# Optimization experiments

Measured on AMD Instinct MI355X. Metric: run time of the kernel, lower is better.

## Reference

```python
import jax, jax.numpy as jnp
import numpy as np

TOP_K = 4

def setup_inputs() -> dict:
    key = jax.random.key(0)
    ks = jax.random.split(key, 10)
    s = 0.02
    return {
        "x": jax.random.normal(ks[0], (4, 1024, 2048), jnp.float32),
        "expert_bias": jnp.zeros((64,), jnp.float32),
        "router_w": jax.random.normal(ks[1], (64, 2048), jnp.float32) * s,
        "gate_w": jax.random.normal(ks[2], (8192, 2048), jnp.float32) * s,
        "up_w": jax.random.normal(ks[3], (8192, 2048), jnp.float32) * s,
        "down_w": jax.random.normal(ks[4], (2048, 8192), jnp.float32) * s,
        "w_down": jax.random.normal(ks[5], (512, 2048), jnp.float32) * s,
        "w_up": jax.random.normal(ks[6], (2048, 512), jnp.float32) * s,
        "experts_w12": jax.random.normal(ks[7], (64, 512, 2048), jnp.float32) * s,
        "experts_w3": jax.random.normal(ks[8], (64, 1024, 512), jnp.float32) * s,
    }


def reference(x, expert_bias, router_w, gate_w, up_w, down_w, w_down, w_up, experts_w12, experts_w3):
    B, S, D = x.shape
    E = router_w.shape[0]
    K = TOP_K
    h = x.reshape(-1, D)            # [N, D]
    N = h.shape[0]
    NK = N * K

    # --- router (fp32) ---
    logits = h @ router_w.T          # [N, E]
    scores = jax.nn.sigmoid(logits)
    z_loss = jnp.mean(logits * logits) * 1e-4
    sel = scores + expert_bias
    _, topk_idx = jax.lax.top_k(sel, K)                      # [N, K]
    topk_logits = jnp.take_along_axis(logits, topk_idx, axis=1)
    gating = jax.nn.softmax(topk_logits, axis=-1)            # [N, K]

    # --- shared SwiGLU expert ---
    shared = (jax.nn.silu(h @ gate_w.T) * (h @ up_w.T)) @ down_w.T   # [N, D]

    # --- bottleneck down projection ---
    hd = h @ w_down.T                # [N, bottle]
    Bn = hd.shape[1]

    # --- dispatch: sort tokens by expert, capacity max_load per expert ---
    flat = topk_idx.reshape(-1)                      # [NK]
    perm = jnp.argsort(flat)                         # stable sort
    sorted_e = flat[perm]
    counts = jnp.bincount(flat, length=E)
    ptr = jnp.cumsum(counts) - counts                # start offset per expert
    local = jnp.arange(NK) - ptr[sorted_e]           # rank within expert
    max_load = (NK // E // 8 + 6) * 8                # static python int
    num_slots = E * max_load
    mask = local < max_load
    slots = sorted_e * max_load + local
    tok = jnp.repeat(jnp.arange(N), K)               # token id per routed slot

    # reverse_map[slot] = token index (N = dummy)
    rm = jnp.full((num_slots + 1,), N, dtype=jnp.int32)
    rm = rm.at[jnp.where(mask, slots, num_slots)].set(tok[perm].astype(jnp.int32))
    reverse_map = rm[:num_slots]

    hwd = jnp.concatenate([hd, jnp.zeros((1, Bn), hd.dtype)], axis=0)
    padding = hwd[reverse_map].reshape(E, max_load, Bn)

    # --- grouped expert GEMMs ---
    h12 = jnp.einsum('emb,ebf->emf', padding, experts_w12)   # [E, L, 2*F]
    h1, h2 = jnp.split(h12, 2, axis=-1)
    pout = jnp.einsum('emf,efb->emb', jax.nn.silu(h1) * h2, experts_w3)
    pout = pout.reshape(-1, Bn)                              # [num_slots, bottle]

    # --- combine: gather back per (token, k) slot and mix with gating ---
    powd = jnp.concatenate([pout, jnp.zeros((1, Bn), pout.dtype)], axis=0)
    gm = jnp.full((NK + 1,), num_slots, dtype=jnp.int32)
    gm = gm.at[jnp.where(mask, perm, NK)].set(jnp.where(mask, slots, num_slots).astype(jnp.int32))
    gather_map = gm[:NK]
    gathered = powd[gather_map].reshape(N, K, Bn)
    routed_b = jnp.einsum('nk,nkb->nb', gating, gathered)
    routed = routed_b @ w_up.T                               # [N, D]

    # eval mode: route_scale = 1.0, moe_scale = 0.5 (one shared expert), aux_loss = 0
    out = (shared + routed) * 0.5
    return out.reshape(B, S, D), z_loss
```

## Files before the change

kernel.cpp:

```cpp
#include <hip/hip_runtime.h>
#include <math.h>

#define NTOK 4096
#define DMODEL 2048
#define ENUM 64
#define HSH 8192
#define BND 512
#define FEXP 1024
#define MAXL 304
#define EPAD 384
#define ECH 16

typedef float f32x4 __attribute__((ext_vector_type(4)));
using bf16x8 = __attribute__((ext_vector_type(8))) __bf16;

typedef const __attribute__((address_space(1))) unsigned int cgu32;
typedef __attribute__((address_space(3))) unsigned int lu32;
#define GLOAD16(g, l) __builtin_amdgcn_global_load_lds((cgu32*)(g), (lu32*)(l), 16, 0, 0)

__device__ __forceinline__ unsigned short f2bf(float f) {
    union { float f; unsigned int u; } v; v.f = f;
    unsigned int u = v.u;
    return (unsigned short)((u + 0x7FFFu + ((u >> 16) & 1u)) >> 16);
}
__device__ __forceinline__ float bf2f(unsigned short s) {
    union { unsigned int u; float f; } v; v.u = ((unsigned int)s) << 16;
    return v.f;
}

__global__ __launch_bounds__(256) void init_kernel(float* zacc, int* slot2tok, unsigned short* hdz) {
    int i = blockIdx.x * 256 + threadIdx.x;
    if (i == 0) *zacc = 0.f;
    if (i < ENUM * MAXL) slot2tok[i] = NTOK;
    if (i < BND) hdz[i] = 0;
}

__global__ __launch_bounds__(256) void convert_kernel(
    const float* __restrict__ in, unsigned short* __restrict__ out, long long n)
{
    long long stride = (long long)gridDim.x * 256 * 8;
    for (long long i = ((long long)blockIdx.x * 256 + threadIdx.x) * 8; i < n; i += stride) {
        float4 a = *(const float4*)(in + i);
        float4 b = *(const float4*)(in + i + 4);
        union { unsigned short s[8]; uint4 v; } o;
        o.s[0] = f2bf(a.x); o.s[1] = f2bf(a.y); o.s[2] = f2bf(a.z); o.s[3] = f2bf(a.w);
        o.s[4] = f2bf(b.x); o.s[5] = f2bf(b.y); o.s[6] = f2bf(b.z); o.s[7] = f2bf(b.w);
        *(uint4*)(out + i) = o.v;
    }
}

__global__ __launch_bounds__(256) void convert_x_kernel(
    const float* __restrict__ in, unsigned short* __restrict__ hi,
    unsigned short* __restrict__ lo, long long n)
{
    long long stride = (long long)gridDim.x * 256 * 8;
    for (long long i = ((long long)blockIdx.x * 256 + threadIdx.x) * 8; i < n; i += stride) {
        float4 a = *(const float4*)(in + i);
        float4 b = *(const float4*)(in + i + 4);
        union { unsigned short s[8]; uint4 v; } oh, ol;
        float f[8] = {a.x, a.y, a.z, a.w, b.x, b.y, b.z, b.w};
#pragma unroll
        for (int j = 0; j < 8; j++) {
            unsigned short h = f2bf(f[j]);
            oh.s[j] = h;
            ol.s[j] = f2bf(f[j] - bf2f(h));
        }
        *(uint4*)(hi + i) = oh.v;
        *(uint4*)(lo + i) = ol.v;
    }
}

__global__ __launch_bounds__(256) void convert_rw_kernel(
    const float* __restrict__ rw, unsigned short* __restrict__ whi,
    unsigned short* __restrict__ wlo)
{
    int i = (blockIdx.x * 256 + threadIdx.x) * 4;
    if (i >= 128 * 2048) return;
    ushort4 oh = {0, 0, 0, 0}, ol = {0, 0, 0, 0};
    if (i < 64 * 2048) {
        float4 f = *(const float4*)(rw + i);
        float v[4] = {f.x, f.y, f.z, f.w};
        unsigned short h;
        h = f2bf(v[0]); oh.x = h; ol.x = f2bf(v[0] - bf2f(h));
        h = f2bf(v[1]); oh.y = h; ol.y = f2bf(v[1] - bf2f(h));
        h = f2bf(v[2]); oh.z = h; ol.z = f2bf(v[2] - bf2f(h));
        h = f2bf(v[3]); oh.w = h; ol.w = f2bf(v[3] - bf2f(h));
    }
    *(ushort4*)(whi + i) = oh;
    *(ushort4*)(wlo + i) = ol;
}

__global__ __launch_bounds__(256) void tconv_kernel(
    const float* __restrict__ in, unsigned short* __restrict__ out, int Kd, int Nd)
{
    __shared__ float t[32][33];
    size_t zoff = (size_t)blockIdx.z * Kd * Nd;
    in += zoff; out += zoff;
    int n0 = blockIdx.x * 32, k0 = blockIdx.y * 32;
    int r = threadIdx.x >> 3, c = (threadIdx.x & 7) * 4;
    float4 v = *(const float4*)(in + (size_t)(k0 + r) * Nd + n0 + c);
    t[r][c] = v.x; t[r][c + 1] = v.y; t[r][c + 2] = v.z; t[r][c + 3] = v.w;
    __syncthreads();
    ushort4 o;
    o.x = f2bf(t[c + 0][r]); o.y = f2bf(t[c + 1][r]);
    o.z = f2bf(t[c + 2][r]); o.w = f2bf(t[c + 3][r]);
    *(ushort4*)(out + (size_t)(n0 + r) * Kd + k0 + c) = o;
}

__global__ __launch_bounds__(256) void rgemm_kernel(
    const unsigned short* __restrict__ xb, const unsigned short* __restrict__ xlo,
    const unsigned short* __restrict__ whi, const unsigned short* __restrict__ wlo,
    float* __restrict__ logits)
{
    __shared__ unsigned short As[2][128 * 64];
    __shared__ unsigned short Bs[2][128 * 64];
    const int z = blockIdx.z;
    const int m0 = blockIdx.y * 128;
    const int tid = threadIdx.x;
    const int lane = tid & 63;
    const int w = tid >> 6;
    const int wm = (w >> 1) * 64;
    const int wn = (w & 1) * 64;

    const unsigned short* Ab = (z == 2) ? xlo : xb;
    const unsigned short* Bb = (z == 1) ? wlo : whi;
    float* Cb = logits + (size_t)z * NTOK * 128;

    size_t asrc[4], bsrc[4];
    int ldso[4];
#pragma unroll
    for (int i = 0; i < 4; i++) {
        int u = i * 256 + tid;
        int r = u >> 3;
        int ce = ((u & 7) ^ (r & 7)) * 8;
        ldso[i] = u * 8;
        asrc[i] = (size_t)(m0 + r) * DMODEL + ce;
        bsrc[i] = (size_t)r * DMODEL + ce;
    }

    const int lrow = lane & 15;
    const int kg = lane >> 4;
    const int mk = (lrow & 7) << 4;
    int arx[4], brx[4];
#pragma unroll
    for (int t = 0; t < 4; t++) {
        arx[t] = (wm + t * 16 + lrow) * 128;
        brx[t] = (wn + t * 16 + lrow) * 128;
    }

    f32x4 acc[4][4];
#pragma unroll
    for (int a = 0; a < 4; a++)
#pragma unroll
        for (int b = 0; b < 4; b++) acc[a][b] = (f32x4)0.f;

#pragma unroll
    for (int i = 0; i < 4; i++) GLOAD16(Ab + asrc[i], &As[0][ldso[i]]);
#pragma unroll
    for (int i = 0; i < 4; i++) GLOAD16(Bb + bsrc[i], &Bs[0][ldso[i]]);
#pragma unroll
    for (int i = 0; i < 4; i++) GLOAD16(Ab + asrc[i] + 64, &As[1][ldso[i]]);
#pragma unroll
    for (int i = 0; i < 4; i++) GLOAD16(Bb + bsrc[i] + 64, &Bs[1][ldso[i]]);

    const int nt = DMODEL >> 6;
    int cur = 0;
    for (int t = 0; t < nt; ++t) {
        if (t + 1 < nt) asm volatile("s_waitcnt vmcnt(8)" ::: "memory");
        else            asm volatile("s_waitcnt vmcnt(0)" ::: "memory");
        __builtin_amdgcn_s_barrier();
        __builtin_amdgcn_sched_barrier(0);
        const char* Abase = (const char*)&As[cur][0];
        const char* Bbase = (const char*)&Bs[cur][0];
#pragma unroll
        for (int ks = 0; ks < 2; ks++) {
            const int cb = (ks * 64 + kg * 16) ^ mk;
            bf16x8 a[4], b[4];
#pragma unroll
            for (int t2 = 0; t2 < 4; t2++) {
                a[t2] = *(const bf16x8*)(Abase + arx[t2] + cb);
                b[t2] = *(const bf16x8*)(Bbase + brx[t2] + cb);
            }
#pragma unroll
            for (int ni = 0; ni < 4; ni++)
#pragma unroll
                for (int mi = 0; mi < 4; mi++)
                    acc[mi][ni] = __builtin_amdgcn_mfma_f32_16x16x32_bf16(a[mi], b[ni], acc[mi][ni], 0, 0, 0);
        }
        __builtin_amdgcn_sched_barrier(0);
        asm volatile("s_waitcnt lgkmcnt(0)" ::: "memory");
        __builtin_amdgcn_s_barrier();
        __builtin_amdgcn_sched_barrier(0);
        const int kn = (t + 2) * 64;
        if (kn < DMODEL) {
#pragma unroll
            for (int i = 0; i < 4; i++) GLOAD16(Ab + asrc[i] + kn, &As[cur][ldso[i]]);
#pragma unroll
            for (int i = 0; i < 4; i++) GLOAD16(Bb + bsrc[i] + kn, &Bs[cur][ldso[i]]);
        }
        cur ^= 1;
    }

    const int rb0 = m0 + wm + (kg << 2);
#pragma unroll
    for (int mi = 0; mi < 4; mi++)
#pragma unroll
        for (int ni = 0; ni < 4; ni++) {
            int col = wn + ni * 16 + lrow;
#pragma unroll
            for (int r = 0; r < 4; r++)
                Cb[(size_t)(rb0 + mi * 16 + r) * 128 + col] = acc[mi][ni][r];
        }
}

__global__ __launch_bounds__(256) void topk_kernel(
    const float* __restrict__ logits, const float* __restrict__ bias,
    int* __restrict__ topk_idx, float* __restrict__ gating, float* __restrict__ zacc)
{
    __shared__ float zpart[4];
    const size_t Z = (size_t)NTOK * 128;
    int wv = threadIdx.x >> 6, lane = threadIdx.x & 63;
    int n = blockIdx.x * 4 + wv;
    const float* lp = logits + (size_t)n * 128 + lane;
    float logit = lp[0] + lp[Z] + lp[2 * Z];
    float sel = 1.f / (1.f + expf(-logit)) + bias[lane];
    float zsq = logit * logit;
    for (int off = 32; off; off >>= 1) zsq += __shfl_down(zsq, off);
    if (lane == 0) zpart[wv] = zsq;
    __syncthreads();
    if (threadIdx.x == 0) atomicAdd(zacc, zpart[0] + zpart[1] + zpart[2] + zpart[3]);
    float cur = sel;
    float ch_logit[4]; int ch_idx[4];
    for (int kk = 0; kk < 4; kk++) {
        float v = cur; int idx = lane;
        for (int off = 1; off < 64; off <<= 1) {
            float v2 = __shfl_xor(v, off);
            int i2 = __shfl_xor(idx, off);
            if (v2 > v || (v2 == v && i2 < idx)) { v = v2; idx = i2; }
        }
        ch_idx[kk] = idx;
        ch_logit[kk] = __shfl(logit, idx);
        if (lane == idx) cur = -1e30f;
    }
    if (lane == 0) {
        float mx = ch_logit[0];
        for (int kk = 1; kk < 4; kk++) mx = fmaxf(mx, ch_logit[kk]);
        float se = 0.f, ex[4];
        for (int kk = 0; kk < 4; kk++) { ex[kk] = expf(ch_logit[kk] - mx); se += ex[kk]; }
        for (int kk = 0; kk < 4; kk++) {
            topk_idx[n * 4 + kk] = ch_idx[kk];
            gating[n * 4 + kk] = ex[kk] / se;
        }
    }
}

__global__ __launch_bounds__(256) void rank_kernel(
    const int* __restrict__ topk_idx, int* __restrict__ slot2tok, int* __restrict__ gmap)
{
    int e = blockIdx.x;
    __shared__ int wsum[4];
    int tid = threadIdx.x;
    int lane = tid & 63, w = tid >> 6;
    int running = 0;
    for (int c = 0; c < NTOK * 4; c += 256) {
        int i = c + tid;
        int fl = topk_idx[i];
        bool m = (fl == e);
        unsigned long long bal = __ballot(m);
        int prefix = __popcll(bal & ((1ULL << lane) - 1ULL));
        if (lane == 0) wsum[w] = __popcll(bal);
        __syncthreads();
        int wbase = 0;
        for (int j = 0; j < w; j++) wbase += wsum[j];
        int total = wsum[0] + wsum[1] + wsum[2] + wsum[3];
        if (m) {
            int rank = running + wbase + prefix;
            int tok = i >> 2;
            if (rank < MAXL) {
                slot2tok[e * MAXL + rank] = tok;
                gmap[i] = e * MAXL + rank;
            } else gmap[i] = -1;
        }
        running += total;
        __syncthreads();
    }
}

template<int GATHER, int EPI>
__global__ __launch_bounds__(256) void gemm2(
    const unsigned short* __restrict__ A, long long aZ, int lda,
    const int* __restrict__ gtab,
    const unsigned short* __restrict__ Bm, long long bZ, int ldb,
    void* __restrict__ Cb, long long cZ, int ldc,
    int M, int K)
{
    __shared__ unsigned short As[2][128 * 64];
    __shared__ unsigned short Bs[2][128 * 64];
    const int z = blockIdx.z;
    const int m0 = blockIdx.y * 128;
    const int n0 = blockIdx.x * 128;
    const int tid = threadIdx.x;
    const int lane = tid & 63;
    const int w = tid >> 6;
    const int wm = (w >> 1) * 64;
    const int wn = (w & 1) * 64;

    const unsigned short* Ab = A + (GATHER ? (size_t)0 : (size_t)z * aZ);
    const unsigned short* Bb = Bm + (size_t)z * bZ;

    size_t asrc[4], bsrc[4];
    int ldso[4];
#pragma unroll
    for (int i = 0; i < 4; i++) {
        int u = i * 256 + tid;
        int r = u >> 3;
        int ce = ((u & 7) ^ (r & 7)) * 8;
        ldso[i] = u * 8;
        if constexpr (GATHER) {
            int mr = m0 + r;
            int tok = (mr < M) ? gtab[(size_t)z * MAXL + mr] : NTOK;
            asrc[i] = (size_t)tok * lda + ce;
        } else {
            asrc[i] = (size_t)(m0 + r) * lda + ce;
        }
        bsrc[i] = (size_t)(n0 + r) * ldb + ce;
    }

    const int lrow = lane & 15;
    const int kg = lane >> 4;
    const int mk = (lrow & 7) << 4;
    int arx[4], brx[4];
#pragma unroll
    for (int t = 0; t < 4; t++) {
        arx[t] = (wm + t * 16 + lrow) * 128;
        brx[t] = (wn + t * 16 + lrow) * 128;
    }

    f32x4 acc[4][4];
#pragma unroll
    for (int a = 0; a < 4; a++)
#pragma unroll
        for (int b = 0; b < 4; b++) acc[a][b] = (f32x4)0.f;

#pragma unroll
    for (int i = 0; i < 4; i++) GLOAD16(Ab + asrc[i], &As[0][ldso[i]]);
#pragma unroll
    for (int i = 0; i < 4; i++) GLOAD16(Bb + bsrc[i], &Bs[0][ldso[i]]);
    if (64 < K) {
#pragma unroll
        for (int i = 0; i < 4; i++) GLOAD16(Ab + asrc[i] + 64, &As[1][ldso[i]]);
#pragma unroll
        for (int i = 0; i < 4; i++) GLOAD16(Bb + bsrc[i] + 64, &Bs[1][ldso[i]]);
    }

    const int nt = K >> 6;
    int cur = 0;
    for (int t = 0; t < nt; ++t) {
        if (t + 1 < nt) asm volatile("s_waitcnt vmcnt(8)" ::: "memory");
        else            asm volatile("s_waitcnt vmcnt(0)" ::: "memory");
        __builtin_amdgcn_s_barrier();
        __builtin_amdgcn_sched_barrier(0);
        const char* Abase = (const char*)&As[cur][0];
        const char* Bbase = (const char*)&Bs[cur][0];
#pragma unroll
        for (int ks = 0; ks < 2; ks++) {
            const int cb = (ks * 64 + kg * 16) ^ mk;
            bf16x8 a[4], b[4];
#pragma unroll
            for (int t2 = 0; t2 < 4; t2++) {
                a[t2] = *(const bf16x8*)(Abase + arx[t2] + cb);
                b[t2] = *(const bf16x8*)(Bbase + brx[t2] + cb);
            }
#pragma unroll
            for (int ni = 0; ni < 4; ni++)
#pragma unroll
                for (int mi = 0; mi < 4; mi++)
                    acc[mi][ni] = __builtin_amdgcn_mfma_f32_16x16x32_bf16(a[mi], b[ni], acc[mi][ni], 0, 0, 0);
        }
        __builtin_amdgcn_sched_barrier(0);
        asm volatile("s_waitcnt lgkmcnt(0)" ::: "memory");
        __builtin_amdgcn_s_barrier();
        __builtin_amdgcn_sched_barrier(0);
        const int kn = (t + 2) * 64;
        if (kn < K) {
#pragma unroll
            for (int i = 0; i < 4; i++) GLOAD16(Ab + asrc[i] + kn, &As[cur][ldso[i]]);
#pragma unroll
            for (int i = 0; i < 4; i++) GLOAD16(Bb + bsrc[i] + kn, &Bs[cur][ldso[i]]);
        }
        cur ^= 1;
    }

    const int rb0 = m0 + wm + (kg << 2);
#pragma unroll
    for (int mi = 0; mi < 4; mi++)
#pragma unroll
        for (int ni = 0; ni < 4; ni++) {
            int col = n0 + wn + ni * 16 + lrow;
#pragma unroll
            for (int r = 0; r < 4; r++) {
                int row = rb0 + mi * 16 + r;
                if (row < M) {
                    size_t ci = (size_t)z * cZ + (size_t)row * ldc + col;
                    float v = acc[mi][ni][r];
                    if constexpr (EPI == 0) {
                        ((unsigned short*)Cb)[ci] = f2bf(v);
                    } else if constexpr (EPI == 1) {
                        unsigned short* cp = (unsigned short*)Cb + ci;
                        float g = bf2f(*cp);
                        *cp = f2bf(g / (1.f + expf(-g)) * v);
                    } else if constexpr (EPI == 2) {
                        ((float*)Cb)[ci] = v;
                    } else {
                        float* cp = (float*)Cb + ci;
                        *cp = (*cp + v) * 0.5f;
                    }
                }
            }
        }
}

__global__ __launch_bounds__(256) void gemmgu(
    const unsigned short* __restrict__ A, int lda,
    const unsigned short* __restrict__ Bg, const unsigned short* __restrict__ Bu,
    int ldb, unsigned short* __restrict__ H, int ldh, int ncol0, int K)
{
    __shared__ unsigned short As[128 * 64];
    __shared__ unsigned short Bgs[128 * 64];
    __shared__ unsigned short Bus[128 * 64];
    const int m0 = blockIdx.y * 128;
    const int n0 = blockIdx.x * 128;
    const int tid = threadIdx.x;
    const int lane = tid & 63;
    const int w = tid >> 6;
    const int wm = (w >> 1) * 64;
    const int wn = (w & 1) * 64;

    size_t asrc[4], bsrc[4];
    int ldso[4];
#pragma unroll
    for (int i = 0; i < 4; i++) {
        int u = i * 256 + tid;
        int r = u >> 3;
        int ce = ((u & 7) ^ (r & 7)) * 8;
        ldso[i] = u * 8;
        asrc[i] = (size_t)(m0 + r) * lda + ce;
        bsrc[i] = (size_t)(n0 + r) * ldb + ce;
    }

    const int lrow = lane & 15;
    const int kg = lane >> 4;
    const int mk = (lrow & 7) << 4;
    int arx[4], brx[4];
#pragma unroll
    for (int t = 0; t < 4; t++) {
        arx[t] = (wm + t * 16 + lrow) * 128;
        brx[t] = (wn + t * 16 + lrow) * 128;
    }

    f32x4 accg[4][4], accu[4][4];
#pragma unroll
    for (int a = 0; a < 4; a++)
#pragma unroll
        for (int b = 0; b < 4; b++) { accg[a][b] = (f32x4)0.f; accu[a][b] = (f32x4)0.f; }

    for (int k0 = 0; k0 < K; k0 += 64) {
#pragma unroll
        for (int i = 0; i < 4; i++) GLOAD16(A + asrc[i] + k0, &As[ldso[i]]);
#pragma unroll
        for (int i = 0; i < 4; i++) GLOAD16(Bg + bsrc[i] + k0, &Bgs[ldso[i]]);
#pragma unroll
        for (int i = 0; i < 4; i++) GLOAD16(Bu + bsrc[i] + k0, &Bus[ldso[i]]);
        __syncthreads();
#pragma unroll
        for (int ks = 0; ks < 2; ks++) {
            const int cb = (ks * 64 + kg * 16) ^ mk;
            bf16x8 a[4], bg[4], bu[4];
#pragma unroll
            for (int t2 = 0; t2 < 4; t2++) {
                a[t2]  = *(const bf16x8*)((const char*)As  + arx[t2] + cb);
                bg[t2] = *(const bf16x8*)((const char*)Bgs + brx[t2] + cb);
                bu[t2] = *(const bf16x8*)((const char*)Bus + brx[t2] + cb);
            }
#pragma unroll
            for (int ni = 0; ni < 4; ni++)
#pragma unroll
                for (int mi = 0; mi < 4; mi++) {
                    accg[mi][ni] = __builtin_amdgcn_mfma_f32_16x16x32_bf16(a[mi], bg[ni], accg[mi][ni], 0, 0, 0);
                    accu[mi][ni] = __builtin_amdgcn_mfma_f32_16x16x32_bf16(a[mi], bu[ni], accu[mi][ni], 0, 0, 0);
                }
        }
        __syncthreads();
    }

    const int rb0 = m0 + wm + (kg << 2);
#pragma unroll
    for (int mi = 0; mi < 4; mi++)
#pragma unroll
        for (int ni = 0; ni < 4; ni++) {
            int col = ncol0 + n0 + wn + ni * 16 + lrow;
#pragma unroll
            for (int r = 0; r < 4; r++) {
                int row = rb0 + mi * 16 + r;
                float g = accg[mi][ni][r];
                float u = accu[mi][ni][r];
                H[(size_t)row * ldh + col] = f2bf(g / (1.f + expf(-g)) * u);
            }
        }
}

__global__ __launch_bounds__(256) void siluact_kernel(
    const unsigned short* __restrict__ h12, unsigned short* __restrict__ act)
{
    int e = blockIdx.y, m = blockIdx.x;
    const unsigned short* hr = h12 + ((size_t)e * EPAD + m) * 2048;
    unsigned short* ar = act + ((size_t)e * EPAD + m) * 1024;
    int j = threadIdx.x * 4;
    ushort4 h1 = *(const ushort4*)(hr + j);
    ushort4 h2 = *(const ushort4*)(hr + 1024 + j);
    ushort4 o;
    float v;
    v = bf2f(h1.x); o.x = f2bf(v / (1.f + expf(-v)) * bf2f(h2.x));
    v = bf2f(h1.y); o.y = f2bf(v / (1.f + expf(-v)) * bf2f(h2.y));
    v = bf2f(h1.z); o.z = f2bf(v / (1.f + expf(-v)) * bf2f(h2.z));
    v = bf2f(h1.w); o.w = f2bf(v / (1.f + expf(-v)) * bf2f(h2.w));
    *(ushort4*)(ar + j) = o;
}

__global__ __launch_bounds__(256) void gather_kernel(
    const unsigned short* __restrict__ pout, const int* __restrict__ gmap,
    const float* __restrict__ gating, unsigned short* __restrict__ routed_b)
{
    int n = blockIdx.x;
    int j = threadIdx.x * 2;
    float a0 = 0.f, a1 = 0.f;
#pragma unroll
    for (int kk = 0; kk < 4; kk++) {
        int slot = gmap[n * 4 + kk];
        float g = gating[n * 4 + kk];
        if (slot >= 0) {
            const unsigned short* pr = pout + (size_t)slot * BND + j;
            a0 += g * bf2f(pr[0]);
            a1 += g * bf2f(pr[1]);
        }
    }
    routed_b[(size_t)n * BND + j] = f2bf(a0);
    routed_b[(size_t)n * BND + j + 1] = f2bf(a1);
}

__global__ void zloss_kernel(const float* zacc, float* out) {
    out[0] = zacc[0] * (1.0e-4f / (float)(NTOK * ENUM));
}

extern "C" void kernel_launch(void* const* d_in, const int* in_sizes, int n_in,
                              void* d_out, int out_size, void* d_ws, size_t ws_size,
                              hipStream_t stream)
{
    const float* x      = (const float*)d_in[0];
    const float* ebias  = (const float*)d_in[1];
    const float* rw     = (const float*)d_in[2];
    const float* gate_w = (const float*)d_in[3];
    const float* up_w   = (const float*)d_in[4];
    const float* down_w = (const float*)d_in[5];
    const float* w_down = (const float*)d_in[6];
    const float* w_up   = (const float*)d_in[7];
    const float* w12    = (const float*)d_in[8];
    const float* w3     = (const float*)d_in[9];
    float* out = (float*)d_out;

    char* ws = (char*)d_ws;
    size_t off = 0;
    auto alloc = [&](size_t b) { size_t o = off; off += (b + 255) & ~(size_t)255; return o; };
    float* zacc     = (float*)(ws + alloc(4));
    int*   topk     = (int*)(ws + alloc((size_t)NTOK * 4 * 4));
    float* gating   = (float*)(ws + alloc((size_t)NTOK * 4 * 4));
    int*   gmap     = (int*)(ws + alloc((size_t)NTOK * 4 * 4));
    int*   slot2tok = (int*)(ws + alloc((size_t)ENUM * MAXL * 4));
    unsigned short* xb     = (unsigned short*)(ws + alloc((size_t)NTOK * DMODEL * 2));
    unsigned short* hd     = (unsigned short*)(ws + alloc((size_t)(NTOK + 1) * BND * 2));
    unsigned short* rb     = (unsigned short*)(ws + alloc((size_t)NTOK * BND * 2));
    unsigned short* wdownb = (unsigned short*)(ws + alloc((size_t)BND * DMODEL * 2));
    unsigned short* wupb   = (unsigned short*)(ws + alloc((size_t)DMODEL * BND * 2));
    unsigned short* wbuf   = (unsigned short*)(ws + alloc((size_t)HSH * DMODEL * 2));
    unsigned short* H1     = (unsigned short*)(ws + alloc((size_t)NTOK * HSH * 2));
    unsigned short* h12  = H1;
    unsigned short* act  = H1 + (size_t)ECH * EPAD * 2048;
    unsigned short* pout = H1 + (size_t)ECH * EPAD * 2048 + (size_t)ECH * EPAD * 1024;
    unsigned short* xlo    = H1;
    float*          logits = (float*)((char*)H1 + (size_t)NTOK * DMODEL * 2);
    unsigned short* whi    = (unsigned short*)((char*)logits + (size_t)3 * NTOK * 128 * 4);
    unsigned short* wlo    = whi + (size_t)128 * DMODEL;

    init_kernel<<<(ENUM * MAXL + 255) / 256, 256, 0, stream>>>(zacc, slot2tok, hd + (size_t)NTOK * BND);

    convert_x_kernel<<<1024, 256, 0, stream>>>(x, xb, xlo, (long long)NTOK * DMODEL);
    convert_rw_kernel<<<(128 * 2048 / 4 + 255) / 256, 256, 0, stream>>>(rw, whi, wlo);
    rgemm_kernel<<<dim3(1, NTOK / 128, 3), 256, 0, stream>>>(xb, xlo, whi, wlo, logits);
    topk_kernel<<<NTOK / 4, 256, 0, stream>>>(logits, ebias, topk, gating, zacc);
    rank_kernel<<<ENUM, 256, 0, stream>>>(topk, slot2tok, gmap);

    convert_kernel<<<256, 256, 0, stream>>>(w_down, wdownb, (long long)BND * DMODEL);
    convert_kernel<<<256, 256, 0, stream>>>(w_up, wupb, (long long)DMODEL * BND);

    gemm2<0, 0><<<dim3(BND / 128, NTOK / 128, 1), 256, 0, stream>>>(
        xb, 0, DMODEL, nullptr, wdownb, 0, DMODEL, hd, 0, BND, NTOK, DMODEL);

    for (int half = 0; half < 2; half++) {
        convert_kernel<<<512, 256, 0, stream>>>(
            gate_w + (size_t)half * (HSH / 2) * DMODEL, wbuf, (long long)(HSH / 2) * DMODEL);
        convert_kernel<<<512, 256, 0, stream>>>(
            up_w + (size_t)half * (HSH / 2) * DMODEL, wbuf + (size_t)(HSH / 2) * DMODEL,
            (long long)(HSH / 2) * DMODEL);
        gemmgu<<<dim3((HSH / 2) / 128, NTOK / 128, 1), 256, 0, stream>>>(
            xb, DMODEL, wbuf, wbuf + (size_t)(HSH / 2) * DMODEL, DMODEL,
            H1, HSH, half * (HSH / 2), DMODEL);
    }
    convert_kernel<<<1024, 256, 0, stream>>>(down_w, wbuf, (long long)DMODEL * HSH);
    gemm2<0, 2><<<dim3(DMODEL / 128, NTOK / 128, 1), 256, 0, stream>>>(
        H1, 0, HSH, nullptr, wbuf, 0, HSH, out, 0, DMODEL, NTOK, HSH);

    for (int c = 0; c < ENUM / ECH; c++) {
        tconv_kernel<<<dim3(2048 / 32, 512 / 32, ECH), 256, 0, stream>>>(
            w12 + (size_t)c * ECH * 512 * 2048, wbuf, 512, 2048);
        gemm2<1, 0><<<dim3(2048 / 128, 3, ECH), 256, 0, stream>>>(
            hd, 0, BND, slot2tok + (size_t)c * ECH * MAXL,
            wbuf, (long long)2048 * 512, 512,
            h12, (long long)EPAD * 2048, 2048, MAXL, BND);
        tconv_kernel<<<dim3(512 / 32, 1024 / 32, ECH), 256, 0, stream>>>(
            w3 + (size_t)c * ECH * 1024 * 512, wbuf, 1024, 512);
        siluact_kernel<<<dim3(EPAD, ECH), 256, 0, stream>>>(h12, act);
        gemm2<0, 0><<<dim3(BND / 128, 3, ECH), 256, 0, stream>>>(
            act, (long long)EPAD * FEXP, FEXP, nullptr,
            wbuf, (long long)BND * FEXP, FEXP,
            pout + (size_t)c * ECH * MAXL * BND, (long long)MAXL * BND, BND, MAXL, FEXP);
    }

    gather_kernel<<<NTOK, 256, 0, stream>>>(pout, gmap, gating, rb);

    gemm2<0, 3><<<dim3(DMODEL / 128, NTOK / 128, 1), 256, 0, stream>>>(
        rb, 0, BND, nullptr, wupb, 0, BND, out, 0, DMODEL, NTOK, BND);

    zloss_kernel<<<1, 1, 0, stream>>>(zacc, out + (size_t)NTOK * DMODEL);
}
```

Before: 1.184 ms.

## Replace shared-expert GEMMs with multi-stage pipelined 128x256 tile kernel

Replaces the gate/up fused GEMM and the down-projection GEMM with a templated kernel that uses 512 threads, a 128x256 output tile and a 3- or 4-deep ring of LDS stages filled by async global-to-LDS loads. Loads for later k-tiles are interleaved with MFMA phases, gated by explicit vmcnt waits and setprio, instead of the previous load-sync-compute-sync loop. The aim is to hide memory latency and raise MFMA utilization on the largest GEMMs. The trade-off is more LDS per block, which lowers occupancy, plus hand-tuned waitcnt counts that must exactly match the number of issued loads.

```diff
diff --git a/kernel.cpp b/kernel.cpp
--- a/kernel.cpp
+++ b/kernel.cpp
@@ -420,77 +420,133 @@
         }
 }
 
-__global__ __launch_bounds__(256) void gemmgu(
+template<int DUAL>
+__global__ __launch_bounds__(512) void gemm6(
     const unsigned short* __restrict__ A, int lda,
-    const unsigned short* __restrict__ Bg, const unsigned short* __restrict__ Bu,
-    int ldb, unsigned short* __restrict__ H, int ldh, int ncol0, int K)
-{
-    __shared__ unsigned short As[128 * 64];
-    __shared__ unsigned short Bgs[128 * 64];
-    __shared__ unsigned short Bus[128 * 64];
+    const unsigned short* __restrict__ B1, const unsigned short* __restrict__ B2, int ldb,
+    void* __restrict__ Cb, int ldc, int ncol0, int K)
+{
+    constexpr int RING = DUAL ? 3 : 4;
+    __shared__ unsigned short As[RING * 128 * 32];
+    __shared__ unsigned short B1s[RING * 256 * 32];
+    __shared__ unsigned short B2s[DUAL ? RING * 256 * 32 : 64];
     const int m0 = blockIdx.y * 128;
-    const int n0 = blockIdx.x * 128;
+    const int n0 = blockIdx.x * 256;
     const int tid = threadIdx.x;
     const int lane = tid & 63;
     const int w = tid >> 6;
-    const int wm = (w >> 1) * 64;
-    const int wn = (w & 1) * 64;
-
-    size_t asrc[4], bsrc[4];
-    int ldso[4];
-#pragma unroll
-    for (int i = 0; i < 4; i++) {
-        int u = i * 256 + tid;
-        int r = u >> 3;
-        int ce = ((u & 7) ^ (r & 7)) * 8;
-        ldso[i] = u * 8;
-        asrc[i] = (size_t)(m0 + r) * lda + ce;
+    const int wm = (w >> 2) * 64;
+    const int wn = (w & 3) * 64;
+
+    size_t asrc;
+    int ldsoA;
+    {
+        int r = tid >> 2;
+        int ce = ((tid & 3) ^ ((r >> 1) & 3)) * 8;
+        ldsoA = tid * 8;
+        asrc = (size_t)(m0 + r) * lda + ce;
+    }
+    size_t bsrc[2];
+    int ldsoB[2];
+#pragma unroll
+    for (int i = 0; i < 2; i++) {
+        int u = i * 512 + tid;
+        int r = u >> 2;
+        int ce = ((u & 3) ^ ((r >> 1) & 3)) * 8;
+        ldsoB[i] = u * 8;
         bsrc[i] = (size_t)(n0 + r) * ldb + ce;
     }
 
     const int lrow = lane & 15;
     const int kg = lane >> 4;
-    const int mk = (lrow & 7) << 4;
+    const int un = (kg ^ ((lrow >> 1) & 3)) << 4;
     int arx[4], brx[4];
 #pragma unroll
-    for (int t = 0; t < 4; t++) {
-        arx[t] = (wm + t * 16 + lrow) * 128;
-        brx[t] = (wn + t * 16 + lrow) * 128;
-    }
-
-    f32x4 accg[4][4], accu[4][4];
+    for (int mi = 0; mi < 4; mi++) arx[mi] = (wm + mi * 16 + lrow) * 64 + un;
+#pragma unroll
+    for (int ni = 0; ni < 4; ni++) brx[ni] = (wn + ni * 16 + lrow) * 64 + un;
+
+    f32x4 acc1[4][4];
+    f32x4 acc2[DUAL ? 4 : 1][DUAL ? 4 : 1];
 #pragma unroll
     for (int a = 0; a < 4; a++)
 #pragma unroll
-        for (int b = 0; b < 4; b++) { accg[a][b] = (f32x4)0.f; accu[a][b] = (f32x4)0.f; }
-
-    for (int k0 = 0; k0 < K; k0 += 64) {
-#pragma unroll
-        for (int i = 0; i < 4; i++) GLOAD16(A + asrc[i] + k0, &As[ldso[i]]);
-#pragma unroll
-        for (int i = 0; i < 4; i++) GLOAD16(Bg + bsrc[i] + k0, &Bgs[ldso[i]]);
-#pragma unroll
-        for (int i = 0; i < 4; i++) GLOAD16(Bu + bsrc[i] + k0, &Bus[ldso[i]]);
-        __syncthreads();
-#pragma unroll
-        for (int ks = 0; ks < 2; ks++) {
-            const int cb = (ks * 64 + kg * 16) ^ mk;
-            bf16x8 a[4], bg[4], bu[4];
-#pragma unroll
-            for (int t2 = 0; t2 < 4; t2++) {
-                a[t2]  = *(const bf16x8*)((const char*)As  + arx[t2] + cb);
-                bg[t2] = *(const bf16x8*)((const char*)Bgs + brx[t2] + cb);
-                bu[t2] = *(const bf16x8*)((const char*)Bus + brx[t2] + cb);
-            }
-#pragma unroll
-            for (int ni = 0; ni < 4; ni++)
-#pragma unroll
-                for (int mi = 0; mi < 4; mi++) {
-                    accg[mi][ni] = __builtin_amdgcn_mfma_f32_16x16x32_bf16(a[mi], bg[ni], accg[mi][ni], 0, 0, 0);
-                    accu[mi][ni] = __builtin_amdgcn_mfma_f32_16x16x32_bf16(a[mi], bu[ni], accu[mi][ni], 0, 0, 0);
-                }
-        }
-        __syncthreads();
+        for (int b = 0; b < 4; b++) {
+            acc1[a][b] = (f32x4)0.f;
+            if constexpr (DUAL) acc2[a][b] = (f32x4)0.f;
+        }
+
+    const int NT = K >> 5;
+    const int PRO = DUAL ? 2 : 3;
+    for (int t = 0; t < PRO && t < NT; ++t) {
+        const int kn = t * 32;
+        unsigned short* as = &As[(t % RING) * 128 * 32];
+        unsigned short* b1s = &B1s[(t % RING) * 256 * 32];
+        GLOAD16(A + asrc + kn, &as[ldsoA]);
+        GLOAD16(B1 + bsrc[0] + kn, &b1s[ldsoB[0]]);
+        GLOAD16(B1 + bsrc[1] + kn, &b1s[ldsoB[1]]);
+        if constexpr (DUAL) {
+            unsigned short* b2s = &B2s[(t % RING) * 256 * 32];
+            GLOAD16(B2 + bsrc[0] + kn, &b2s[ldsoB[0]]);
+            GLOAD16(B2 + bsrc[1] + kn, &b2s[ldsoB[1]]);
+        }
+    }
+
+    for (int kt = 0; kt < NT; ++kt) {
+        if constexpr (DUAL) {
+            if (kt + 1 < NT) asm volatile("s_waitcnt vmcnt(5)" ::: "memory");
+            else             asm volatile("s_waitcnt vmcnt(0)" ::: "memory");
+        } else {
+            if (kt + 2 < NT)       asm volatile("s_waitcnt vmcnt(6)" ::: "memory");
+            else if (kt + 1 < NT)  asm volatile("s_waitcnt vmcnt(3)" ::: "memory");
+            else                   asm volatile("s_waitcnt vmcnt(0)" ::: "memory");
+        }
+        __builtin_amdgcn_s_barrier();
+        __builtin_amdgcn_sched_barrier(0);
+
+        const int slot = kt % RING;
+        const char* Ab = (const char*)&As[slot * 128 * 32];
+        const char* Bb1 = (const char*)&B1s[slot * 256 * 32];
+        const char* Bb2 = DUAL ? (const char*)&B2s[slot * 256 * 32] : nullptr;
+
+        const int tstage = kt + (DUAL ? 2 : 3);
+        const bool pf = (tstage < NT);
+        const int sslot = tstage % RING;
+        const int kn = tstage * 32;
+        unsigned short* sas = &As[sslot * 128 * 32];
+        unsigned short* sb1 = &B1s[sslot * 256 * 32];
+        unsigned short* sb2 = DUAL ? &B2s[sslot * 256 * 32] : nullptr;
+
+        bf16x8 b1[4], b2[DUAL ? 4 : 1];
+#pragma unroll
+        for (int ni = 0; ni < 4; ni++) {
+            b1[ni] = *(const bf16x8*)(Bb1 + brx[ni]);
+            if constexpr (DUAL) b2[ni] = *(const bf16x8*)(Bb2 + brx[ni]);
+        }
+
+#define G6_PHASE(q, GL)                                                              \
+        {                                                                            \
+            bf16x8 af = *(const bf16x8*)(Ab + arx[q]);                               \
+            GL;                                                                      \
+            __builtin_amdgcn_s_setprio(1);                                           \
+            _Pragma("unroll")                                                        \
+            for (int ni = 0; ni < 4; ni++) {                                         \
+                acc1[q][ni] = __builtin_amdgcn_mfma_f32_16x16x32_bf16(               \
+                    af, b1[ni], acc1[q][ni], 0, 0, 0);                               \
+                if constexpr (DUAL)                                                  \
+                    acc2[q][ni] = __builtin_amdgcn_mfma_f32_16x16x32_bf16(           \
+                        af, b2[ni], acc2[q][ni], 0, 0, 0);                           \
+            }                                                                        \
+            __builtin_amdgcn_s_setprio(0);                                           \
+            __builtin_amdgcn_sched_barrier(0);                                       \
+        }
+
+        G6_PHASE(0, if (pf) GLOAD16(A + asrc + kn, &sas[ldsoA]))
+        G6_PHASE(1, if (pf) GLOAD16(B1 + bsrc[0] + kn, &sb1[ldsoB[0]]))
+        G6_PHASE(2, if (pf) { GLOAD16(B1 + bsrc[1] + kn, &sb1[ldsoB[1]]);
+                              if constexpr (DUAL) GLOAD16(B2 + bsrc[0] + kn, &sb2[ldsoB[0]]); })
+        G6_PHASE(3, if (pf) { if constexpr (DUAL) GLOAD16(B2 + bsrc[1] + kn, &sb2[ldsoB[1]]); })
+#undef G6_PHASE
     }
 
     const int rb0 = m0 + wm + (kg << 2);
@@ -502,9 +558,14 @@
 #pragma unroll
             for (int r = 0; r < 4; r++) {
                 int row = rb0 + mi * 16 + r;
-                float g = accg[mi][ni][r];
-                float u = accu[mi][ni][r];
-                H[(size_t)row * ldh + col] = f2bf(g / (1.f + expf(-g)) * u);
+                if constexpr (DUAL) {
+                    float g = acc1[mi][ni][r];
+                    float u = acc2[mi][ni][r];
+                    ((unsigned short*)Cb)[(size_t)row * ldc + col] =
+                        f2bf(g / (1.f + expf(-g)) * u);
+                } else {
+                    ((float*)Cb)[(size_t)row * ldc + col] = acc1[mi][ni][r];
+                }
             }
         }
 }
@@ -611,13 +672,13 @@
         convert_kernel<<<512, 256, 0, stream>>>(
             up_w + (size_t)half * (HSH / 2) * DMODEL, wbuf + (size_t)(HSH / 2) * DMODEL,
             (long long)(HSH / 2) * DMODEL);
-        gemmgu<<<dim3((HSH / 2) / 128, NTOK / 128, 1), 256, 0, stream>>>(
+        gemm6<1><<<dim3((HSH / 2) / 256, NTOK / 128), 512, 0, stream>>>(
             xb, DMODEL, wbuf, wbuf + (size_t)(HSH / 2) * DMODEL, DMODEL,
             H1, HSH, half * (HSH / 2), DMODEL);
     }
     convert_kernel<<<1024, 256, 0, stream>>>(down_w, wbuf, (long long)DMODEL * HSH);
-    gemm2<0, 2><<<dim3(DMODEL / 128, NTOK / 128, 1), 256, 0, stream>>>(
-        H1, 0, HSH, nullptr, wbuf, 0, HSH, out, 0, DMODEL, NTOK, HSH);
+    gemm6<0><<<dim3(DMODEL / 256, NTOK / 128), 512, 0, stream>>>(
+        H1, HSH, wbuf, nullptr, HSH, out, DMODEL, 0, HSH);
 
     for (int c = 0; c < ENUM / ECH; c++) {
         tconv_kernel<<<dim3(2048 / 32, 512 / 32, ECH), 256, 0, stream>>>(
```

Measured after the change: 1.083 ms. 8.5% less time.
